# Kernel optimization log

Measured on AMD Instinct MI355X. Metric: run time of the kernel, lower is better.

Reference implementation:

```python
import jax, jax.numpy as jnp
import numpy as np

N_OBJ = 8        # objects per sample -> nc2 = 28 pair-nodes per sample (code caps nc2 < 30)
MAX_REL = 10     # relations per sample (num_rel is uniform so total_rels is static)


def setup_inputs() -> dict:
    key = jax.random.key(0)
    k1, k2, k3, k4, k5 = jax.random.split(key, 5)
    B, D, n = 1024, 512, N_OBJ
    iu, ju = np.triu_indices(n, k=1)                     # (i<j) pair layout, lexicographic
    nc2 = iu.shape[0]                                     # 28
    bcol = np.repeat(np.arange(B), nc2)
    slicing_tensor = jnp.asarray(
        np.stack([bcol, np.tile(iu, B), np.tile(ju, B)], axis=1), dtype=jnp.int32)  # [B*nc2, 3]
    spatial_branch_feature_map = jax.random.normal(k1, (B * nc2, D), dtype=jnp.float32)
    W_self = jax.random.normal(k2, (D, D), dtype=jnp.float32) / np.float32(np.sqrt(D))
    W_nbr = jax.random.normal(k3, (D, D), dtype=jnp.float32) / np.float32(np.sqrt(D))
    b = jnp.zeros((D,), dtype=jnp.float32)
    # object_pairs: distinct indices in [0, n)
    i0 = jax.random.randint(k4, (B, MAX_REL), 0, n)
    off = jax.random.randint(k5, (B, MAX_REL), 1, n)
    i1 = (i0 + off) % n
    object_pairs = jnp.stack([i0, i1], axis=-1).astype(jnp.int32)  # [B, MAX_REL, 2]
    num_rel = jnp.full((B,), MAX_REL, dtype=jnp.int32)
    num_obj = jnp.full((B,), n, dtype=jnp.int32)
    return {"spatial_branch_feature_map": spatial_branch_feature_map, "W_self": W_self,
            "W_nbr": W_nbr, "b": b, "slicing_tensor": slicing_tensor,
            "object_pairs": object_pairs, "num_rel": num_rel, "num_obj": num_obj}


def reference(spatial_branch_feature_map, W_self, W_nbr, b,
              slicing_tensor, object_pairs, num_rel, num_obj):
    x = spatial_branch_feature_map
    N, D = x.shape
    B = num_obj.shape[0]
    nc2 = N // B                                          # pair-nodes per sample
    n = N_OBJ
    # --- fully-connected edge index per sample (incl. self-loops), offset per batch ---
    src_l = jnp.repeat(jnp.arange(nc2, dtype=jnp.int32), nc2)   # row0: t1 outer loop
    dst_l = jnp.tile(jnp.arange(nc2, dtype=jnp.int32), nc2)     # row1: t2 inner loop
    offs = (jnp.arange(B, dtype=jnp.int32) * nc2)[:, None]
    src = (src_l[None, :] + offs).reshape(-1)                   # [B*nc2^2]
    dst = (dst_l[None, :] + offs).reshape(-1)
    # --- GNN layer: sum-aggregate neighbor messages, linear + ReLU ---
    agg = jax.ops.segment_sum(x[src], dst, num_segments=N)      # [N, D]
    h = jax.nn.relu(x @ W_self + agg @ W_nbr + b)               # [N, D]
    # --- key-matching gather (replaces nested python-loop boolean matching) ---
    keys = slicing_tensor[:, 0] * (n * n) + slicing_tensor[:, 1] * n + slicing_tensor[:, 2]
    lut = jnp.zeros((B * n * n,), dtype=jnp.int32).at[keys].set(jnp.arange(N, dtype=jnp.int32))
    pmin = jnp.minimum(object_pairs[..., 0], object_pairs[..., 1])
    pmax = jnp.maximum(object_pairs[..., 0], object_pairs[..., 1])
    bidx = jnp.arange(B, dtype=jnp.int32)[:, None]
    rel_keys = (bidx * (n * n) + pmin * n + pmax).reshape(-1)   # [B*MAX_REL]
    rows = lut[rel_keys]
    return h[rows]                                              # [total_rels, D]
```

## Files before the change

### kernel.cpp

```cpp
#include <hip/hip_runtime.h>
#include <hip/hip_bf16.h>
#include <stdint.h>


typedef __bf16 bf16_t;
typedef __bf16 bf16x8 __attribute__((ext_vector_type(8)));
typedef __bf16 bf16x2 __attribute__((ext_vector_type(2)));
typedef float  f32x4  __attribute__((ext_vector_type(4)));

#define D_DIM 512
#define NC2   28
#define NOBJ  8
#define MAXREL 10
#define B_SAMP 1024
#define OUTROWS (B_SAMP * MAXREL)

__device__ __forceinline__ void gload_lds16(const void* g, void* l) {
  __builtin_amdgcn_global_load_lds(
      (const __attribute__((address_space(1))) unsigned int*)g,
      (__attribute__((address_space(3))) unsigned int*)l, 16, 0, 0);
}

__global__ __launch_bounds__(256) void prep_kernel(
    const float* __restrict__ x, const float* __restrict__ Wself,
    const float* __restrict__ Wnbr, const int* __restrict__ pairs,
    bf16_t* __restrict__ Sbf, bf16_t* __restrict__ Abf,
    bf16_t* __restrict__ Wst, bf16_t* __restrict__ Wnt)
{
  const int blk = blockIdx.x, tid = threadIdx.x;
  if (blk < B_SAMP) {
    __shared__ int rel_row[MAXREL];
    if (tid < MAXREL) {
      int p0 = pairs[blk * MAXREL * 2 + tid * 2 + 0];
      int p1 = pairs[blk * MAXREL * 2 + tid * 2 + 1];
      int pmin = min(p0, p1), pmax = max(p0, p1);
      rel_row[tid] = 7 * pmin - (pmin * (pmin - 1)) / 2 + (pmax - pmin - 1);
    }
    __syncthreads();
    int rr[MAXREL];
    #pragma unroll
    for (int j = 0; j < MAXREL; ++j) rr[j] = rel_row[j];

    const float2* xr = (const float2*)(x + (size_t)blk * NC2 * D_DIM);
    float2 a = {0.f, 0.f};
    #pragma unroll
    for (int r = 0; r < NC2; ++r) {
      float2 v = xr[r * (D_DIM / 2) + tid];
      a.x += v.x; a.y += v.y;
      bf16x2 o = { (bf16_t)v.x, (bf16_t)v.y };
      #pragma unroll
      for (int j = 0; j < MAXREL; ++j)
        if (rr[j] == r)
          *(bf16x2*)(Abf + (size_t)(blk * MAXREL + j) * D_DIM + tid * 2) = o;
    }
    bf16x2 o = { (bf16_t)a.x, (bf16_t)a.y };
    *(bf16x2*)(Sbf + (size_t)blk * D_DIM + tid * 2) = o;
  } else {
    __shared__ float tile[32][33];
    const int t = blk - B_SAMP;
    const float* W  = (t & 256) ? Wnbr : Wself;
    bf16_t*     Wt  = (t & 256) ? Wnt  : Wst;
    const int r = t & 255;
    const int k0 = (r & 15) * 32, n0 = (r >> 4) * 32;
    const int tx = tid & 31, ty = tid >> 5;
    #pragma unroll
    for (int i = 0; i < 32; i += 8)
      tile[ty + i][tx] = W[(size_t)(k0 + ty + i) * D_DIM + n0 + tx];
    __syncthreads();
    #pragma unroll
    for (int i = 0; i < 32; i += 8)
      Wt[(size_t)(n0 + ty + i) * D_DIM + k0 + tx] = (bf16_t)tile[tx][ty + i];
  }
}

#define SA_BYTES 6144
#define SB_BYTES 16384
__global__ __launch_bounds__(256) void fused_gemm_kernel(
    const bf16_t* __restrict__ Abf, const bf16_t* __restrict__ Sbf,
    const bf16_t* __restrict__ Wst, const bf16_t* __restrict__ Wnt,
    const float* __restrict__ bias, float* __restrict__ out)
{
  __shared__ __align__(16) unsigned char pool[2 * SA_BYTES + 2 * SB_BYTES];

  const int tid = threadIdx.x;
  const int w = tid >> 6, l = tid & 63;
  const int kg = l >> 4, lr = l & 15;
  const int n0 = blockIdx.y * 128;
  const int arow0 = blockIdx.x * 80;
  const int srow0 = blockIdx.x * 8;

  f32x4 acc[6][2] = {};

  auto STAGE = [&](int bsel, int k0) {
    bf16_t* aB = (bf16_t*)(pool + bsel * SA_BYTES);
    bf16_t* bB = (bf16_t*)(pool + 2 * SA_BYTES + bsel * SB_BYTES);
    #pragma unroll
    for (int r = 0; r < 6; ++r) {
      int slot = r * 4 + w;
      if (slot < 6) {
        int c = slot * 64 + l;
        int row = c >> 2, ch = c & 3;
        int sch = ch ^ ((row >> 1) & 3);
        const bf16_t* g = (slot < 5)
            ? Abf + (size_t)(arow0 + row) * D_DIM + k0 + sch * 8
            : Sbf + (size_t)(srow0 + (row & 7)) * D_DIM + k0 + sch * 8;
        gload_lds16(g, aB + (size_t)slot * 512);
      } else if (slot < 22) {
        int c = (slot - 6) * 64 + l;
        int mat = c >> 9, rc = c & 511;
        int row = rc >> 2, ch = rc & 3;
        int sch = ch ^ ((row >> 1) & 3);
        const bf16_t* W = mat ? Wnt : Wst;
        gload_lds16(W + (size_t)(n0 + row) * D_DIM + k0 + sch * 8,
                    bB + (size_t)(slot - 6) * 512);
      }
    }
  };

  STAGE(0, 0);
  __syncthreads();

  const int xorc = (kg ^ ((lr >> 1) & 3)) * 8;
  int cur = 0;
  #pragma unroll 2
  for (int t = 0; t < 16; ++t) {
    if (t < 15) STAGE(cur ^ 1, (t + 1) * 32);

    const bf16_t* aC = (const bf16_t*)(pool + cur * SA_BYTES);
    const bf16_t* bC = (const bf16_t*)(pool + 2 * SA_BYTES + cur * SB_BYTES);
    bf16x8 af[6], bs[2], bn[2];
    #pragma unroll
    for (int s = 0; s < 6; ++s)
      af[s] = *(const bf16x8*)(aC + (s * 16 + lr) * 32 + xorc);
    #pragma unroll
    for (int u = 0; u < 2; ++u) {
      bs[u] = *(const bf16x8*)(bC + (w * 32 + u * 16 + lr) * 32 + xorc);
      bn[u] = *(const bf16x8*)(bC + 4096 + (w * 32 + u * 16 + lr) * 32 + xorc);
    }
    #pragma unroll
    for (int s = 0; s < 5; ++s)
      #pragma unroll
      for (int u = 0; u < 2; ++u)
        acc[s][u] = __builtin_amdgcn_mfma_f32_16x16x32_bf16(af[s], bs[u], acc[s][u], 0, 0, 0);
    #pragma unroll
    for (int u = 0; u < 2; ++u)
      acc[5][u] = __builtin_amdgcn_mfma_f32_16x16x32_bf16(af[5], bn[u], acc[5][u], 0, 0, 0);

    __syncthreads();
    cur ^= 1;
  }

  float* Tt = (float*)pool;
  #pragma unroll
  for (int u = 0; u < 2; ++u)
    #pragma unroll
    for (int reg = 0; reg < 4; ++reg)
      Tt[(kg * 4 + reg) * 132 + w * 32 + u * 16 + lr] = acc[5][u][reg];
  __syncthreads();

  const float bv0 = bias[n0 + w * 32 + lr];
  const float bv1 = bias[n0 + w * 32 + 16 + lr];
  #pragma unroll
  for (int s = 0; s < 5; ++s) {
    #pragma unroll
    for (int u = 0; u < 2; ++u) {
      #pragma unroll
      for (int reg = 0; reg < 4; ++reg) {
        int rloc = s * 16 + kg * 4 + reg;
        int ls = rloc / MAXREL;
        int c = w * 32 + u * 16 + lr;
        float v = acc[s][u][reg] + Tt[ls * 132 + c] + (u ? bv1 : bv0);
        out[(size_t)(arow0 + rloc) * D_DIM + n0 + c] = fmaxf(v, 0.0f);
      }
    }
  }
}

extern "C" void kernel_launch(void* const* d_in, const int* in_sizes, int n_in,
                              void* d_out, int out_size, void* d_ws, size_t ws_size,
                              hipStream_t stream) {
  const float* x     = (const float*)d_in[0];
  const float* Wself = (const float*)d_in[1];
  const float* Wnbr  = (const float*)d_in[2];
  const float* bias  = (const float*)d_in[3];
  const int*   pairs = (const int*)d_in[5];

  char* ws = (char*)d_ws;
  size_t off = 0;
  bf16_t* Sbf = (bf16_t*)(ws + off); off += (size_t)B_SAMP * D_DIM * 2;
  bf16_t* Wst = (bf16_t*)(ws + off); off += (size_t)D_DIM * D_DIM * 2;
  bf16_t* Wnt = (bf16_t*)(ws + off); off += (size_t)D_DIM * D_DIM * 2;
  bf16_t* Abf = (bf16_t*)(ws + off); off += (size_t)OUTROWS * D_DIM * 2;

  prep_kernel<<<B_SAMP + 512, 256, 0, stream>>>(
      x, Wself, Wnbr, pairs, Sbf, Abf, Wst, Wnt);
  fused_gemm_kernel<<<dim3(OUTROWS / 80, D_DIM / 128), 256, 0, stream>>>(
      Abf, Sbf, Wst, Wnt, bias, (float*)d_out);
}
```

Baseline: 36.44 us.

## Load GEMM fragments directly from global into registers, dropping LDS staging

The GEMM kernel no longer stages A and W tiles through double-buffered shared memory with per-iteration barriers. Each lane now loads its MFMA fragments straight from global memory into registers, ping-ponging two register sets so the next k-step's loads overlap the current MFMAs. Shared memory is kept only for the small epilogue exchange of the per-sample neighbor term. The aim is to remove LDS traffic and the barriers, but weight tiles are no longer shared across the four waves, so global/L2 traffic and register pressure go up.

```diff
diff --git a/kernel.cpp b/kernel.cpp
--- a/kernel.cpp
+++ b/kernel.cpp
@@ -14,12 +14,6 @@
 #define MAXREL 10
 #define B_SAMP 1024
 #define OUTROWS (B_SAMP * MAXREL)
-
-__device__ __forceinline__ void gload_lds16(const void* g, void* l) {
-  __builtin_amdgcn_global_load_lds(
-      (const __attribute__((address_space(1))) unsigned int*)g,
-      (__attribute__((address_space(3))) unsigned int*)l, 16, 0, 0);
-}
 
 __global__ __launch_bounds__(256) void prep_kernel(
     const float* __restrict__ x, const float* __restrict__ Wself,
@@ -73,93 +67,71 @@
   }
 }
 
-#define SA_BYTES 6144
-#define SB_BYTES 16384
+#define LOADF(A, B, k) do {                                                   \
+    _Pragma("unroll")                                                         \
+    for (int s_ = 0; s_ < 6; ++s_)                                            \
+      A[s_] = *(const bf16x8*)(pA[s_] + (k) * 32);                            \
+    B[0] = *(const bf16x8*)(pB0 + (k) * 32);                                  \
+    B[1] = *(const bf16x8*)(pB1 + (k) * 32);                                  \
+    B[2] = *(const bf16x8*)(pN0 + (k) * 32);                                  \
+    B[3] = *(const bf16x8*)(pN1 + (k) * 32);                                  \
+  } while (0)
+
+#define DOMFMA(A, B) do {                                                     \
+    _Pragma("unroll")                                                         \
+    for (int s_ = 0; s_ < 5; ++s_) {                                          \
+      acc[s_][0] = __builtin_amdgcn_mfma_f32_16x16x32_bf16(A[s_], B[0], acc[s_][0], 0, 0, 0); \
+      acc[s_][1] = __builtin_amdgcn_mfma_f32_16x16x32_bf16(A[s_], B[1], acc[s_][1], 0, 0, 0); \
+    }                                                                         \
+    acc[5][0] = __builtin_amdgcn_mfma_f32_16x16x32_bf16(A[5], B[2], acc[5][0], 0, 0, 0); \
+    acc[5][1] = __builtin_amdgcn_mfma_f32_16x16x32_bf16(A[5], B[3], acc[5][1], 0, 0, 0); \
+  } while (0)
+
 __global__ __launch_bounds__(256) void fused_gemm_kernel(
     const bf16_t* __restrict__ Abf, const bf16_t* __restrict__ Sbf,
     const bf16_t* __restrict__ Wst, const bf16_t* __restrict__ Wnt,
     const float* __restrict__ bias, float* __restrict__ out)
 {
-  __shared__ __align__(16) unsigned char pool[2 * SA_BYTES + 2 * SB_BYTES];
+  __shared__ float Tex[4][16][33];
 
   const int tid = threadIdx.x;
   const int w = tid >> 6, l = tid & 63;
   const int kg = l >> 4, lr = l & 15;
-  const int n0 = blockIdx.y * 128;
+  const int n0 = blockIdx.y * 128 + w * 32;
   const int arow0 = blockIdx.x * 80;
   const int srow0 = blockIdx.x * 8;
 
+  const bf16_t* pA[6];
+  #pragma unroll
+  for (int s = 0; s < 5; ++s)
+    pA[s] = Abf + (size_t)(arow0 + s * 16 + lr) * D_DIM + kg * 8;
+  pA[5] = Sbf + (size_t)(srow0 + (lr & 7)) * D_DIM + kg * 8;
+  const bf16_t* pB0 = Wst + (size_t)(n0 + lr) * D_DIM + kg * 8;
+  const bf16_t* pB1 = Wst + (size_t)(n0 + 16 + lr) * D_DIM + kg * 8;
+  const bf16_t* pN0 = Wnt + (size_t)(n0 + lr) * D_DIM + kg * 8;
+  const bf16_t* pN1 = Wnt + (size_t)(n0 + 16 + lr) * D_DIM + kg * 8;
+
   f32x4 acc[6][2] = {};
+  bf16x8 aX[6], bX[4], aY[6], bY[4];
 
-  auto STAGE = [&](int bsel, int k0) {
-    bf16_t* aB = (bf16_t*)(pool + bsel * SA_BYTES);
-    bf16_t* bB = (bf16_t*)(pool + 2 * SA_BYTES + bsel * SB_BYTES);
-    #pragma unroll
-    for (int r = 0; r < 6; ++r) {
-      int slot = r * 4 + w;
-      if (slot < 6) {
-        int c = slot * 64 + l;
-        int row = c >> 2, ch = c & 3;
-        int sch = ch ^ ((row >> 1) & 3);
-        const bf16_t* g = (slot < 5)
-            ? Abf + (size_t)(arow0 + row) * D_DIM + k0 + sch * 8
-            : Sbf + (size_t)(srow0 + (row & 7)) * D_DIM + k0 + sch * 8;
-        gload_lds16(g, aB + (size_t)slot * 512);
-      } else if (slot < 22) {
-        int c = (slot - 6) * 64 + l;
-        int mat = c >> 9, rc = c & 511;
-        int row = rc >> 2, ch = rc & 3;
-        int sch = ch ^ ((row >> 1) & 3);
-        const bf16_t* W = mat ? Wnt : Wst;
-        gload_lds16(W + (size_t)(n0 + row) * D_DIM + k0 + sch * 8,
-                    bB + (size_t)(slot - 6) * 512);
-      }
-    }
-  };
-
-  STAGE(0, 0);
-  __syncthreads();
-
-  const int xorc = (kg ^ ((lr >> 1) & 3)) * 8;
-  int cur = 0;
-  #pragma unroll 2
-  for (int t = 0; t < 16; ++t) {
-    if (t < 15) STAGE(cur ^ 1, (t + 1) * 32);
-
-    const bf16_t* aC = (const bf16_t*)(pool + cur * SA_BYTES);
-    const bf16_t* bC = (const bf16_t*)(pool + 2 * SA_BYTES + cur * SB_BYTES);
-    bf16x8 af[6], bs[2], bn[2];
-    #pragma unroll
-    for (int s = 0; s < 6; ++s)
-      af[s] = *(const bf16x8*)(aC + (s * 16 + lr) * 32 + xorc);
-    #pragma unroll
-    for (int u = 0; u < 2; ++u) {
-      bs[u] = *(const bf16x8*)(bC + (w * 32 + u * 16 + lr) * 32 + xorc);
-      bn[u] = *(const bf16x8*)(bC + 4096 + (w * 32 + u * 16 + lr) * 32 + xorc);
-    }
-    #pragma unroll
-    for (int s = 0; s < 5; ++s)
-      #pragma unroll
-      for (int u = 0; u < 2; ++u)
-        acc[s][u] = __builtin_amdgcn_mfma_f32_16x16x32_bf16(af[s], bs[u], acc[s][u], 0, 0, 0);
-    #pragma unroll
-    for (int u = 0; u < 2; ++u)
-      acc[5][u] = __builtin_amdgcn_mfma_f32_16x16x32_bf16(af[5], bn[u], acc[5][u], 0, 0, 0);
-
-    __syncthreads();
-    cur ^= 1;
+  LOADF(aX, bX, 0);
+  #pragma unroll
+  for (int t = 0; t < 16; t += 2) {
+    if (t + 1 < 16) LOADF(aY, bY, t + 1);
+    DOMFMA(aX, bX);
+    if (t + 2 < 16) LOADF(aX, bX, t + 2);
+    DOMFMA(aY, bY);
   }
 
-  float* Tt = (float*)pool;
   #pragma unroll
   for (int u = 0; u < 2; ++u)
     #pragma unroll
     for (int reg = 0; reg < 4; ++reg)
-      Tt[(kg * 4 + reg) * 132 + w * 32 + u * 16 + lr] = acc[5][u][reg];
+      Tex[w][kg * 4 + reg][u * 16 + lr] = acc[5][u][reg];
   __syncthreads();
 
-  const float bv0 = bias[n0 + w * 32 + lr];
-  const float bv1 = bias[n0 + w * 32 + 16 + lr];
+  const float bv0 = bias[n0 + lr];
+  const float bv1 = bias[n0 + 16 + lr];
   #pragma unroll
   for (int s = 0; s < 5; ++s) {
     #pragma unroll
@@ -168,8 +140,8 @@
       for (int reg = 0; reg < 4; ++reg) {
         int rloc = s * 16 + kg * 4 + reg;
         int ls = rloc / MAXREL;
-        int c = w * 32 + u * 16 + lr;
-        float v = acc[s][u][reg] + Tt[ls * 132 + c] + (u ? bv1 : bv0);
+        int c = u * 16 + lr;
+        float v = acc[s][u][reg] + Tex[w][ls][c] + (u ? bv1 : bv0);
         out[(size_t)(arow0 + rloc) * D_DIM + n0 + c] = fmaxf(v, 0.0f);
       }
     }
```

Result: slower. 58.94 us (+61.8%).

## Fuse prep and GEMM into one cooperative kernel with grid sync

Applied to the files above, without the earlier changes.

Merges the conversion/gather prep kernel and the fused GEMM into a single cooperative launch of 512 blocks separated by a grid-wide barrier. The prep phase now handles two samples per block with float4 loads, and each block also transposes one weight tile. The GEMM pipeline swaps __syncthreads for explicit vmcnt waits plus raw barriers, raises MFMA priority with s_setprio, and fully unrolls the K loop. This aims to remove the gap between the two kernel launches and cut tail effects, at the cost of grid-sync overhead and a fallback to two launches if the cooperative launch fails.

```diff
diff --git a/kernel.cpp b/kernel.cpp
--- a/kernel.cpp
+++ b/kernel.cpp
@@ -1,11 +1,14 @@
 #include <hip/hip_runtime.h>
 #include <hip/hip_bf16.h>
+#include <hip/hip_cooperative_groups.h>
 #include <stdint.h>
+
+namespace cg = cooperative_groups;
 
 
 typedef __bf16 bf16_t;
 typedef __bf16 bf16x8 __attribute__((ext_vector_type(8)));
-typedef __bf16 bf16x2 __attribute__((ext_vector_type(2)));
+typedef __bf16 bf16x4 __attribute__((ext_vector_type(4)));
 typedef float  f32x4  __attribute__((ext_vector_type(4)));
 
 #define D_DIM 512
@@ -15,79 +18,96 @@
 #define B_SAMP 1024
 #define OUTROWS (B_SAMP * MAXREL)
 
+#define SA_BYTES 6144
+#define SB_BYTES 16384
+#define POOL_BYTES (2 * (SA_BYTES + SB_BYTES))
+
 __device__ __forceinline__ void gload_lds16(const void* g, void* l) {
   __builtin_amdgcn_global_load_lds(
       (const __attribute__((address_space(1))) unsigned int*)g,
       (__attribute__((address_space(3))) unsigned int*)l, 16, 0, 0);
 }
 
-__global__ __launch_bounds__(256) void prep_kernel(
+__device__ __forceinline__ void phaseA_body(
+    unsigned char* pool, int bid, int tid,
     const float* __restrict__ x, const float* __restrict__ Wself,
     const float* __restrict__ Wnbr, const int* __restrict__ pairs,
     bf16_t* __restrict__ Sbf, bf16_t* __restrict__ Abf,
     bf16_t* __restrict__ Wst, bf16_t* __restrict__ Wnt)
 {
-  const int blk = blockIdx.x, tid = threadIdx.x;
-  if (blk < B_SAMP) {
-    __shared__ int rel_row[MAXREL];
-    if (tid < MAXREL) {
-      int p0 = pairs[blk * MAXREL * 2 + tid * 2 + 0];
-      int p1 = pairs[blk * MAXREL * 2 + tid * 2 + 1];
-      int pmin = min(p0, p1), pmax = max(p0, p1);
-      rel_row[tid] = 7 * pmin - (pmin * (pmin - 1)) / 2 + (pmax - pmin - 1);
-    }
+  int*    rr     = (int*)pool;
+  float4* oddsum = (float4*)(pool + 128);
+  float*  tile   = (float*)(pool + 128 + 4096);
+
+  if (tid < 2 * MAXREL) {
+    int sm = bid * 2 + tid / MAXREL, j = tid % MAXREL;
+    int p0 = pairs[sm * MAXREL * 2 + j * 2 + 0];
+    int p1 = pairs[sm * MAXREL * 2 + j * 2 + 1];
+    int pmin = min(p0, p1), pmax = max(p0, p1);
+    rr[tid] = 7 * pmin - (pmin * (pmin - 1)) / 2 + (pmax - pmin - 1);
+  }
+  __syncthreads();
+
+  const int h = tid >> 7, c = tid & 127;
+  const int sm0 = bid * 2;
+  const float4* x40 = (const float4*)(x + (size_t)sm0 * NC2 * D_DIM);
+  const float4* x41 = x40 + NC2 * 128;
+
+  float4 a0 = {0.f,0.f,0.f,0.f}, a1 = {0.f,0.f,0.f,0.f};
+  #pragma unroll
+  for (int rp = 0; rp < NC2 / 2; ++rp) {
+    float4 v0 = x40[(rp * 2 + h) * 128 + c];
+    float4 v1 = x41[(rp * 2 + h) * 128 + c];
+    a0.x += v0.x; a0.y += v0.y; a0.z += v0.z; a0.w += v0.w;
+    a1.x += v1.x; a1.y += v1.y; a1.z += v1.z; a1.w += v1.w;
+  }
+  if (h) { oddsum[c] = a0; oddsum[128 + c] = a1; }
+  __syncthreads();
+  if (!h) {
+    float4 b0 = oddsum[c], b1 = oddsum[128 + c];
+    bf16x4 o0 = { (bf16_t)(a0.x + b0.x), (bf16_t)(a0.y + b0.y),
+                  (bf16_t)(a0.z + b0.z), (bf16_t)(a0.w + b0.w) };
+    bf16x4 o1 = { (bf16_t)(a1.x + b1.x), (bf16_t)(a1.y + b1.y),
+                  (bf16_t)(a1.z + b1.z), (bf16_t)(a1.w + b1.w) };
+    *(bf16x4*)(Sbf + (size_t)sm0 * D_DIM + c * 4) = o0;
+    *(bf16x4*)(Sbf + (size_t)(sm0 + 1) * D_DIM + c * 4) = o1;
+  }
+  #pragma unroll
+  for (int j = h; j < MAXREL; j += 2) {
+    float4 v0 = x40[rr[j] * 128 + c];
+    float4 v1 = x41[rr[10 + j] * 128 + c];
+    bf16x4 o0 = { (bf16_t)v0.x, (bf16_t)v0.y, (bf16_t)v0.z, (bf16_t)v0.w };
+    bf16x4 o1 = { (bf16_t)v1.x, (bf16_t)v1.y, (bf16_t)v1.z, (bf16_t)v1.w };
+    *(bf16x4*)(Abf + (size_t)(sm0 * MAXREL + j) * D_DIM + c * 4) = o0;
+    *(bf16x4*)(Abf + (size_t)((sm0 + 1) * MAXREL + j) * D_DIM + c * 4) = o1;
+  }
+  {
+    int mat = bid >> 8, pc = bid & 255;
+    int k0 = (pc & 15) * 32, n1 = (pc >> 4) * 32;
+    const float* W  = mat ? Wnbr : Wself;
+    bf16_t*      Wt = mat ? Wnt  : Wst;
+    int tx = tid & 31, ty = tid >> 5;
+    #pragma unroll
+    for (int i = 0; i < 32; i += 8)
+      tile[(ty + i) * 33 + tx] = W[(size_t)(k0 + ty + i) * D_DIM + n1 + tx];
     __syncthreads();
-    int rr[MAXREL];
-    #pragma unroll
-    for (int j = 0; j < MAXREL; ++j) rr[j] = rel_row[j];
-
-    const float2* xr = (const float2*)(x + (size_t)blk * NC2 * D_DIM);
-    float2 a = {0.f, 0.f};
-    #pragma unroll
-    for (int r = 0; r < NC2; ++r) {
-      float2 v = xr[r * (D_DIM / 2) + tid];
-      a.x += v.x; a.y += v.y;
-      bf16x2 o = { (bf16_t)v.x, (bf16_t)v.y };
-      #pragma unroll
-      for (int j = 0; j < MAXREL; ++j)
-        if (rr[j] == r)
-          *(bf16x2*)(Abf + (size_t)(blk * MAXREL + j) * D_DIM + tid * 2) = o;
-    }
-    bf16x2 o = { (bf16_t)a.x, (bf16_t)a.y };
-    *(bf16x2*)(Sbf + (size_t)blk * D_DIM + tid * 2) = o;
-  } else {
-    __shared__ float tile[32][33];
-    const int t = blk - B_SAMP;
-    const float* W  = (t & 256) ? Wnbr : Wself;
-    bf16_t*     Wt  = (t & 256) ? Wnt  : Wst;
-    const int r = t & 255;
-    const int k0 = (r & 15) * 32, n0 = (r >> 4) * 32;
-    const int tx = tid & 31, ty = tid >> 5;
     #pragma unroll
     for (int i = 0; i < 32; i += 8)
-      tile[ty + i][tx] = W[(size_t)(k0 + ty + i) * D_DIM + n0 + tx];
-    __syncthreads();
-    #pragma unroll
-    for (int i = 0; i < 32; i += 8)
-      Wt[(size_t)(n0 + ty + i) * D_DIM + k0 + tx] = (bf16_t)tile[tx][ty + i];
-  }
-}
-
-#define SA_BYTES 6144
-#define SB_BYTES 16384
-__global__ __launch_bounds__(256) void fused_gemm_kernel(
+      Wt[(size_t)(n1 + ty + i) * D_DIM + k0 + tx] = (bf16_t)tile[tx * 33 + ty + i];
+  }
+}
+
+__device__ __forceinline__ void phaseB_body(
+    unsigned char* pool, int bid, int tid,
     const bf16_t* __restrict__ Abf, const bf16_t* __restrict__ Sbf,
     const bf16_t* __restrict__ Wst, const bf16_t* __restrict__ Wnt,
     const float* __restrict__ bias, float* __restrict__ out)
 {
-  __shared__ __align__(16) unsigned char pool[2 * SA_BYTES + 2 * SB_BYTES];
-
-  const int tid = threadIdx.x;
   const int w = tid >> 6, l = tid & 63;
   const int kg = l >> 4, lr = l & 15;
-  const int n0 = blockIdx.y * 128;
-  const int arow0 = blockIdx.x * 80;
-  const int srow0 = blockIdx.x * 8;
+  const int bx = bid & 127, by = bid >> 7;
+  const int n0 = by * 128;
+  const int arow0 = bx * 80, srow0 = bx * 8;
 
   f32x4 acc[6][2] = {};
 
@@ -98,64 +118,73 @@
     for (int r = 0; r < 6; ++r) {
       int slot = r * 4 + w;
       if (slot < 6) {
-        int c = slot * 64 + l;
-        int row = c >> 2, ch = c & 3;
+        int cch = slot * 64 + l;
+        int row = cch >> 2, ch = cch & 3;
         int sch = ch ^ ((row >> 1) & 3);
-        const bf16_t* g = (slot < 5)
+        const bf16_t* g = (row < 80)
             ? Abf + (size_t)(arow0 + row) * D_DIM + k0 + sch * 8
             : Sbf + (size_t)(srow0 + (row & 7)) * D_DIM + k0 + sch * 8;
-        gload_lds16(g, aB + (size_t)slot * 512);
+        gload_lds16(g, aB + (size_t)cch * 8);
       } else if (slot < 22) {
-        int c = (slot - 6) * 64 + l;
-        int mat = c >> 9, rc = c & 511;
+        int cch = (slot - 6) * 64 + l;
+        int mat = cch >> 9, rc = cch & 511;
         int row = rc >> 2, ch = rc & 3;
         int sch = ch ^ ((row >> 1) & 3);
         const bf16_t* W = mat ? Wnt : Wst;
         gload_lds16(W + (size_t)(n0 + row) * D_DIM + k0 + sch * 8,
-                    bB + (size_t)(slot - 6) * 512);
+                    bB + (size_t)cch * 8);
       }
     }
   };
 
   STAGE(0, 0);
-  __syncthreads();
+  asm volatile("s_waitcnt vmcnt(0)" ::: "memory");
+  __builtin_amdgcn_s_barrier();
 
   const int xorc = (kg ^ ((lr >> 1) & 3)) * 8;
   int cur = 0;
-  #pragma unroll 2
+  #pragma unroll
   for (int t = 0; t < 16; ++t) {
-    if (t < 15) STAGE(cur ^ 1, (t + 1) * 32);
+    if (t < 15) {
+      STAGE(cur ^ 1, (t + 1) * 32);
+      if (w < 2) asm volatile("s_waitcnt vmcnt(6)" ::: "memory");
+      else       asm volatile("s_waitcnt vmcnt(5)" ::: "memory");
+    } else {
+      asm volatile("s_waitcnt vmcnt(0)" ::: "memory");
+    }
+    __builtin_amdgcn_s_barrier();
 
     const bf16_t* aC = (const bf16_t*)(pool + cur * SA_BYTES);
     const bf16_t* bC = (const bf16_t*)(pool + 2 * SA_BYTES + cur * SB_BYTES);
-    bf16x8 af[6], bs[2], bn[2];
+    bf16x8 af[6], bsf[2], bnf[2];
     #pragma unroll
     for (int s = 0; s < 6; ++s)
       af[s] = *(const bf16x8*)(aC + (s * 16 + lr) * 32 + xorc);
     #pragma unroll
     for (int u = 0; u < 2; ++u) {
-      bs[u] = *(const bf16x8*)(bC + (w * 32 + u * 16 + lr) * 32 + xorc);
-      bn[u] = *(const bf16x8*)(bC + 4096 + (w * 32 + u * 16 + lr) * 32 + xorc);
-    }
+      bsf[u] = *(const bf16x8*)(bC + (w * 32 + u * 16 + lr) * 32 + xorc);
+      bnf[u] = *(const bf16x8*)(bC + 4096 + (w * 32 + u * 16 + lr) * 32 + xorc);
+    }
+    __builtin_amdgcn_s_setprio(1);
     #pragma unroll
     for (int s = 0; s < 5; ++s)
       #pragma unroll
       for (int u = 0; u < 2; ++u)
-        acc[s][u] = __builtin_amdgcn_mfma_f32_16x16x32_bf16(af[s], bs[u], acc[s][u], 0, 0, 0);
-    #pragma unroll
-    for (int u = 0; u < 2; ++u)
-      acc[5][u] = __builtin_amdgcn_mfma_f32_16x16x32_bf16(af[5], bn[u], acc[5][u], 0, 0, 0);
-
-    __syncthreads();
+        acc[s][u] = __builtin_amdgcn_mfma_f32_16x16x32_bf16(af[s], bsf[u], acc[s][u], 0, 0, 0);
+    acc[5][0] = __builtin_amdgcn_mfma_f32_16x16x32_bf16(af[5], bnf[0], acc[5][0], 0, 0, 0);
+    acc[5][1] = __builtin_amdgcn_mfma_f32_16x16x32_bf16(af[5], bnf[1], acc[5][1], 0, 0, 0);
+    __builtin_amdgcn_s_setprio(0);
+
+    __builtin_amdgcn_s_barrier();
     cur ^= 1;
   }
 
-  float* Tt = (float*)pool;
+  float* Tex = (float*)pool;
   #pragma unroll
   for (int u = 0; u < 2; ++u)
     #pragma unroll
     for (int reg = 0; reg < 4; ++reg)
-      Tt[(kg * 4 + reg) * 132 + w * 32 + u * 16 + lr] = acc[5][u][reg];
+      Tex[(w * 16 + kg * 4 + reg) * 33 + u * 16 + lr] = acc[5][u][reg];
   __syncthreads();
 
   const float bv0 = bias[n0 + w * 32 + lr];
@@ -168,12 +197,41 @@
       for (int reg = 0; reg < 4; ++reg) {
         int rloc = s * 16 + kg * 4 + reg;
         int ls = rloc / MAXREL;
-        int c = w * 32 + u * 16 + lr;
-        float v = acc[s][u][reg] + Tt[ls * 132 + c] + (u ? bv1 : bv0);
-        out[(size_t)(arow0 + rloc) * D_DIM + n0 + c] = fmaxf(v, 0.0f);
+        int cc = u * 16 + lr;
+        float v = acc[s][u][reg] + Tex[(w * 16 + ls) * 33 + cc] + (u ? bv1 : bv0);
+        out[(size_t)(arow0 + rloc) * D_DIM + n0 + w * 32 + cc] = fmaxf(v, 0.0f);
       }
     }
   }
+}
+
+__global__ __launch_bounds__(256, 2) void fused_all_kernel(
+    const float* x, const float* Wself, const float* Wnbr,
+    const float* bias, const int* pairs,
+    bf16_t* Sbf, bf16_t* Abf, bf16_t* Wst, bf16_t* Wnt, float* out)
+{
+  __shared__ __align__(16) unsigned char pool[POOL_BYTES];
+  phaseA_body(pool, blockIdx.x, threadIdx.x, x, Wself, Wnbr, pairs,
+              Sbf, Abf, Wst, Wnt);
+  cg::this_grid().sync();
+  phaseB_body(pool, blockIdx.x, threadIdx.x, Abf, Sbf, Wst, Wnt, bias, out);
+}
+
+__global__ __launch_bounds__(256) void prepA_kernel(
+    const float* x, const float* Wself, const float* Wnbr, const int* pairs,
+    bf16_t* Sbf, bf16_t* Abf, bf16_t* Wst, bf16_t* Wnt)
+{
+  __shared__ __align__(16) unsigned char pool[16384];
+  phaseA_body(pool, blockIdx.x, threadIdx.x, x, Wself, Wnbr, pairs,
+              Sbf, Abf, Wst, Wnt);
+}
+
+__global__ __launch_bounds__(256, 2) void gemmB_kernel(
+    const bf16_t* Abf, const bf16_t* Sbf, const bf16_t* Wst,
+    const bf16_t* Wnt, const float* bias, float* out)
+{
+  __shared__ __align__(16) unsigned char pool[POOL_BYTES];
+  phaseB_body(pool, blockIdx.x, threadIdx.x, Abf, Sbf, Wst, Wnt, bias, out);
 }
 
 extern "C" void kernel_launch(void* const* d_in, const int* in_sizes, int n_in,
@@ -191,9 +249,16 @@
   bf16_t* Wst = (bf16_t*)(ws + off); off += (size_t)D_DIM * D_DIM * 2;
   bf16_t* Wnt = (bf16_t*)(ws + off); off += (size_t)D_DIM * D_DIM * 2;
   bf16_t* Abf = (bf16_t*)(ws + off); off += (size_t)OUTROWS * D_DIM * 2;
-
-  prep_kernel<<<B_SAMP + 512, 256, 0, stream>>>(
-      x, Wself, Wnbr, pairs, Sbf, Abf, Wst, Wnt);
-  fused_gemm_kernel<<<dim3(OUTROWS / 80, D_DIM / 128), 256, 0, stream>>>(
-      Abf, Sbf, Wst, Wnt, bias, (float*)d_out);
-}
+  float*  outp = (float*)d_out;
+
+  void* args[] = { (void*)&x, (void*)&Wself, (void*)&Wnbr, (void*)&bias,
+                   (void*)&pairs, (void*)&Sbf, (void*)&Abf, (void*)&Wst,
+                   (void*)&Wnt, (void*)&outp };
+  hipError_t e = hipLaunchCooperativeKernel(
+      (const void*)fused_all_kernel, dim3(512), dim3(256), args, 0, stream);
+  if (e != hipSuccess) {
+    prepA_kernel<<<512, 256, 0, stream>>>(x, Wself, Wnbr, pairs,
+                                          Sbf, Abf, Wst, Wnt);
+    gemmB_kernel<<<512, 256, 0, stream>>>(Abf, Sbf, Wst, Wnt, bias, outp);
+  }
+}
```

Result: slower. 110.5 us (+203.1%).
